# Kernel optimization log

Measured on AMD Instinct MI355X. Metric: run time of the kernel, lower is better.

Reference implementation:

```python
import jax, jax.numpy as jnp
import numpy as np

DIRECTIONS = [(0, 0), (1, 0), (-1, 0), (0, 1), (0, -1)]  # (dx, dy)
BN_EPS = 1e-5


def shift2d(x, directions=DIRECTIONS):
    # x: (B, C, H, W). Split channels into G groups, roll each spatially,
    # zero out the wrapped-around border (zero_pad mode), then concat.
    C = x.shape[1]
    G = len(directions)
    base = C // G
    sizes = [base] * (G - 1) + [C - base * (G - 1)]
    starts = np.concatenate([[0], np.cumsum(sizes)])
    out = []
    for i, (dx, dy) in enumerate(directions):
        chunk = x[:, starts[i]:starts[i + 1]]
        if dx == 0 and dy == 0:
            out.append(chunk)
            continue
        y = jnp.roll(chunk, shift=(dy, dx), axis=(-2, -1))
        if dy > 0:
            y = y.at[..., :dy, :].set(0.0)
        elif dy < 0:
            y = y.at[..., dy:, :].set(0.0)
        if dx > 0:
            y = y.at[..., :, :dx].set(0.0)
        elif dx < 0:
            y = y.at[..., :, dx:].set(0.0)
        out.append(y)
    return jnp.concatenate(out, axis=1)


def setup_inputs() -> dict:
    key = jax.random.key(0)
    k1, k2, k3, k4 = jax.random.split(key, 4)
    B, Cin, Cout, H, W = 32, 256, 256, 56, 56
    x = jax.random.normal(k1, (B, Cin, H, W), dtype=jnp.float32)
    pw_w = jax.random.normal(k2, (Cout, Cin), dtype=jnp.float32) * (1.0 / np.sqrt(Cin))
    gamma = jnp.ones((Cout,), dtype=jnp.float32)
    beta = jnp.zeros((Cout,), dtype=jnp.float32)
    running_mean = jax.random.normal(k3, (Cout,), dtype=jnp.float32) * 0.1
    running_var = jax.random.uniform(k4, (Cout,), dtype=jnp.float32, minval=0.5, maxval=1.5)
    return {"x": x, "pw_w": pw_w, "gamma": gamma, "beta": beta,
            "running_mean": running_mean, "running_var": running_var}


def reference(x, pw_w, gamma, beta, running_mean, running_var):
    # Shift (parameter-free spatial mixing)
    y = shift2d(x)
    # stride=1 -> down is Identity
    # 1x1 conv (no bias): pointwise channel mixing
    y = jnp.einsum('bchw,oc->bohw', y, pw_w)
    # BatchNorm2d (inference form with running stats) + ReLU
    inv = gamma * jax.lax.rsqrt(running_var + BN_EPS)
    y = y * inv[None, :, None, None] + (beta - running_mean * inv)[None, :, None, None]
    return jax.nn.relu(y)
```

## Files before the change

kernel.cpp:

```cpp
#include <hip/hip_runtime.h>

#define H_ 56
#define W_ 56
#define HW_ 3136
#define CIN_ 256
#define COUT_ 256

typedef __attribute__((ext_vector_type(8))) short short8;
typedef __attribute__((ext_vector_type(4))) float f32x4;

__device__ unsigned short g_wbf[COUT_ * CIN_];

__device__ __forceinline__ int swz32(int n) { return ((n ^ (n >> 3)) & 3) << 3; }

__device__ __forceinline__ unsigned short f2bf(float f) {
  union { float f; unsigned int i; } v; v.f = f;
  unsigned int b = v.i + (0x7fffu + ((v.i >> 16) & 1u));
  return (unsigned short)(b >> 16);
}

__device__ __forceinline__ void gload_lds16(const unsigned short* g, unsigned short* l) {
  __builtin_amdgcn_global_load_lds(
      (const __attribute__((address_space(1))) unsigned int*)g,
      (__attribute__((address_space(3))) unsigned int*)l, 16, 0, 0);
}

__device__ __forceinline__ void shift_decode(int c, int& dx, int& dy) {
  if (c < 102)      { dy = 0; dx = (c < 51) ? 0 : 1; }
  else if (c < 153) { dx = -1; dy = 0; }
  else if (c < 204) { dx = 0;  dy = 1; }
  else              { dx = 0;  dy = -1; }
}

__global__ __launch_bounds__(256)
void prep_weights(const float* __restrict__ wgt) {
  int idx  = blockIdx.x * 256 + threadIdx.x;
  int tile = idx >> 12;
  int bm = tile >> 3, kt = tile & 7;
  int e   = idx & 4095;
  int m   = e >> 5, col = e & 31;
  int o   = bm * 128 + m;
  int k   = kt * 32 + (col ^ swz32(m));
  g_wbf[idx] = f2bf(wgt[o * CIN_ + k]);
}

__global__ __launch_bounds__(256, 4)
void shiftconv_gemm(const float* __restrict__ x,
                    const float* __restrict__ gamma,
                    const float* __restrict__ beta,
                    const float* __restrict__ rmean,
                    const float* __restrict__ rvar,
                    float* __restrict__ out)
{
  __shared__ unsigned short Alds[2][128 * 32];
  __shared__ unsigned short Blds[2][64 * 32];
  __shared__ float bnp[256];

  const int t = threadIdx.x;
  const int orig = blockIdx.x;
  const int wgid = (orig & 7) * 392 + (orig >> 3);
  const int bm   = wgid & 1;
  const int bn   = wgid >> 1;

  const int lane = t & 63;
  const int wv   = t >> 6;
  const int wm   = wv >> 1;
  const int wn   = wv & 1;
  const int quad = lane >> 4;
  const int l15  = lane & 15;

  if (t < 128) {
    int o = bm * 128 + t;
    float inv = gamma[o] * rsqrtf(rvar[o] + 1e-5f);
    bnp[2 * t]     = inv;
    bnp[2 * t + 1] = beta[o] - rmean[o] * inv;
  }

  const int nl    = t & 63;
  const int kk    = (t >> 6) * 8;
  const int nglob = bn * 64 + nl;
  const int bidx  = nglob / HW_;
  const int rem   = nglob - bidx * HW_;
  const int hh    = rem / W_;
  const int ww    = rem - hh * W_;
  const size_t xb = (size_t)bidx * CIN_ * HW_;
  unsigned short* bdst0 = &Blds[0][nl * 32 + (kk ^ swz32(nl))];
  unsigned short* bdst1 = &Blds[1][nl * 32 + (kk ^ swz32(nl))];

  const unsigned short* wsrc = g_wbf + bm * (8 * 4096) + t * 8;

  f32x4 acc[4][2];
  #pragma unroll
  for (int i = 0; i < 4; ++i)
    #pragma unroll
    for (int j = 0; j < 2; ++j)
      acc[i][j] = (f32x4){0.f, 0.f, 0.f, 0.f};

  float fv[8];

  auto loadB = [&](int ktile) {
    #pragma unroll
    for (int j = 0; j < 8; ++j) {
      int c = ktile * 32 + kk + j;
      int dx, dy; shift_decode(c, dx, dy);
      int h2 = hh - dy, w2 = ww - dx;
      float v = 0.f;
      if ((unsigned)h2 < (unsigned)H_ && (unsigned)w2 < (unsigned)W_)
        v = x[xb + (size_t)c * HW_ + h2 * W_ + w2];
      fv[j] = v;
    }
  };
  auto writeB = [&](unsigned short* dst) {
    union { short8 v; unsigned short s[8]; } pk;
    #pragma unroll
    for (int j = 0; j < 8; ++j) pk.s[j] = f2bf(fv[j]);
    *(short8*)dst = pk.v;
  };

  {
    const unsigned short* g = wsrc;
    gload_lds16(g,        &Alds[0][wv * 512]);
    gload_lds16(g + 2048, &Alds[0][wv * 512 + 2048]);
  }
  loadB(0);
  writeB(bdst0);
  __syncthreads();

  const int kb = quad * 8;
  int buf = 0;

  for (int kt = 0; kt < 8; ++kt) {
    if (kt < 7) {
      const unsigned short* g = wsrc + (kt + 1) * 4096;
      gload_lds16(g,        &Alds[buf ^ 1][wv * 512]);
      gload_lds16(g + 2048, &Alds[buf ^ 1][wv * 512 + 2048]);
      loadB(kt + 1);
    }

    short8 af[4], bfr[2];
    #pragma unroll
    for (int f = 0; f < 4; ++f) {
      int ml = wm * 64 + f * 16 + l15;
      af[f] = *(const short8*)(&Alds[buf][ml * 32 + (kb ^ swz32(ml))]);
    }
    #pragma unroll
    for (int g2 = 0; g2 < 2; ++g2) {
      int nl2 = wn * 32 + g2 * 16 + l15;
      bfr[g2] = *(const short8*)(&Blds[buf][nl2 * 32 + (kb ^ swz32(nl2))]);
    }
    #pragma unroll
    for (int mf = 0; mf < 4; ++mf)
      #pragma unroll
      for (int nf = 0; nf < 2; ++nf)
        acc[mf][nf] = __builtin_amdgcn_mfma_f32_16x16x32_bf16(
            af[mf], bfr[nf], acc[mf][nf], 0, 0, 0);

    if (kt < 7)
      writeB((buf ^ 1) ? bdst1 : bdst0);

    __syncthreads();
    buf ^= 1;
  }

  size_t nbase[2];
  #pragma unroll
  for (int nf = 0; nf < 2; ++nf) {
    int ng  = bn * 64 + wn * 32 + nf * 16 + l15;
    int b2  = ng / HW_;
    int hw2 = ng - b2 * HW_;
    nbase[nf] = (size_t)b2 * COUT_ * HW_ + hw2;
  }
  #pragma unroll
  for (int mf = 0; mf < 4; ++mf) {
    int mloc = wm * 64 + mf * 16 + quad * 4;
    float inv[4], add[4];
    #pragma unroll
    for (int r = 0; r < 4; ++r) {
      inv[r] = bnp[2 * (mloc + r)];
      add[r] = bnp[2 * (mloc + r) + 1];
    }
    size_t obase = (size_t)(bm * 128 + mloc) * HW_;
    #pragma unroll
    for (int nf = 0; nf < 2; ++nf) {
      #pragma unroll
      for (int r = 0; r < 4; ++r) {
        float v = fmaf(acc[mf][nf][r], inv[r], add[r]);
        out[nbase[nf] + obase + (size_t)r * HW_] = fmaxf(v, 0.0f);
      }
    }
  }
}

extern "C" void kernel_launch(void* const* d_in, const int* in_sizes, int n_in,
                              void* d_out, int out_size, void* d_ws, size_t ws_size,
                              hipStream_t stream) {
  const float* x     = (const float*)d_in[0];
  const float* wgt   = (const float*)d_in[1];
  const float* gamma = (const float*)d_in[2];
  const float* beta  = (const float*)d_in[3];
  const float* rmean = (const float*)d_in[4];
  const float* rvar  = (const float*)d_in[5];
  float* out = (float*)d_out;

  prep_weights<<<dim3(256), dim3(256), 0, stream>>>(wgt);
  shiftconv_gemm<<<dim3(3136), dim3(256), 0, stream>>>(x, gamma, beta, rmean, rvar, out);
}
```

Measured before the change: 210.7 us.

## Double K tile to 64, restructure shifted B loads with precomputed masks

```diff
diff --git a/kernel.cpp b/kernel.cpp
--- a/kernel.cpp
+++ b/kernel.cpp
@@ -11,8 +11,6 @@
 
 __device__ unsigned short g_wbf[COUT_ * CIN_];
 
-__device__ __forceinline__ int swz32(int n) { return ((n ^ (n >> 3)) & 3) << 3; }
-
 __device__ __forceinline__ unsigned short f2bf(float f) {
   union { float f; unsigned int i; } v; v.f = f;
   unsigned int b = v.i + (0x7fffu + ((v.i >> 16) & 1u));
@@ -25,26 +23,26 @@
       (__attribute__((address_space(3))) unsigned int*)l, 16, 0, 0);
 }
 
-__device__ __forceinline__ void shift_decode(int c, int& dx, int& dy) {
-  if (c < 102)      { dy = 0; dx = (c < 51) ? 0 : 1; }
-  else if (c < 153) { dx = -1; dy = 0; }
-  else if (c < 204) { dx = 0;  dy = 1; }
-  else              { dx = 0;  dy = -1; }
-}
-
 __global__ __launch_bounds__(256)
 void prep_weights(const float* __restrict__ wgt) {
-  int idx  = blockIdx.x * 256 + threadIdx.x;
-  int tile = idx >> 12;
-  int bm = tile >> 3, kt = tile & 7;
-  int e   = idx & 4095;
-  int m   = e >> 5, col = e & 31;
+  int idx = blockIdx.x * 256 + threadIdx.x;
+  int bm  = idx >> 15;
+  int kt  = (idx >> 13) & 3;
+  int e   = idx & 8191;
+  int m   = e >> 6;
+  int u   = (e >> 3) & 7;
+  int j   = e & 7;
   int o   = bm * 128 + m;
-  int k   = kt * 32 + (col ^ swz32(m));
+  int k   = kt * 64 + (((u ^ (m & 7)) << 3) | j);
   g_wbf[idx] = f2bf(wgt[o * CIN_ + k]);
 }
 
-__global__ __launch_bounds__(256, 4)
+__device__ __forceinline__ float shload(const float* __restrict__ p, bool m, int off) {
+  float v = p[m ? off : 0];
+  return m ? v : 0.f;
+}
+
+__global__ __launch_bounds__(256, 3)
 void shiftconv_gemm(const float* __restrict__ x,
                     const float* __restrict__ gamma,
                     const float* __restrict__ beta,
@@ -52,8 +50,8 @@
                     const float* __restrict__ rvar,
                     float* __restrict__ out)
 {
-  __shared__ unsigned short Alds[2][128 * 32];
-  __shared__ unsigned short Blds[2][64 * 32];
+  __shared__ unsigned short Alds[2][128 * 64];
+  __shared__ unsigned short Blds[2][64 * 64];
   __shared__ float bnp[256];
 
   const int t = threadIdx.x;
@@ -77,17 +75,23 @@
   }
 
   const int nl    = t & 63;
-  const int kk    = (t >> 6) * 8;
+  const int kg    = __builtin_amdgcn_readfirstlane(t >> 6);
+  const int kg16  = kg << 4;
   const int nglob = bn * 64 + nl;
   const int bidx  = nglob / HW_;
   const int rem   = nglob - bidx * HW_;
   const int hh    = rem / W_;
   const int ww    = rem - hh * W_;
-  const size_t xb = (size_t)bidx * CIN_ * HW_;
-  unsigned short* bdst0 = &Blds[0][nl * 32 + (kk ^ swz32(nl))];
-  unsigned short* bdst1 = &Blds[1][nl * 32 + (kk ^ swz32(nl))];
-
-  const unsigned short* wsrc = g_wbf + bm * (8 * 4096) + t * 8;
+  const float* __restrict__ px = x + (size_t)bidx * CIN_ * HW_ + hh * W_ + ww;
+  const bool mL = (ww >= 1);
+  const bool mR = (ww <= W_ - 2);
+  const bool mU = (hh >= 1);
+  const bool mD = (hh <= H_ - 2);
+  const int  h7 = nl & 7;
+  unsigned short* const bpA = &Blds[0][nl * 64];
+  unsigned short* const bpB = &Blds[1][nl * 64];
+
+  const unsigned short* wsrc = g_wbf + bm * 32768 + t * 8;
 
   f32x4 acc[4][2];
   #pragma unroll
@@ -96,67 +100,76 @@
     for (int j = 0; j < 2; ++j)
       acc[i][j] = (f32x4){0.f, 0.f, 0.f, 0.f};
 
-  float fv[8];
-
-  auto loadB = [&](int ktile) {
-    #pragma unroll
-    for (int j = 0; j < 8; ++j) {
-      int c = ktile * 32 + kk + j;
-      int dx, dy; shift_decode(c, dx, dy);
-      int h2 = hh - dy, w2 = ww - dx;
-      float v = 0.f;
-      if ((unsigned)h2 < (unsigned)H_ && (unsigned)w2 < (unsigned)W_)
-        v = x[xb + (size_t)c * HW_ + h2 * W_ + w2];
+  float fv[16];
+
+  auto loadB = [&](int kt4) {
+    #pragma unroll
+    for (int j = 0; j < 16; ++j) {
+      int c = kt4 * 64 + kg16 + j;
+      const float* p = px + (size_t)c * HW_;
+      float v;
+      if (c < 51)       v = p[0];
+      else if (c < 102) v = shload(p, mL, -1);
+      else if (c < 153) v = shload(p, mR, +1);
+      else if (c < 204) v = shload(p, mU, -W_);
+      else              v = shload(p, mD, +W_);
       fv[j] = v;
     }
   };
-  auto writeB = [&](unsigned short* dst) {
-    union { short8 v; unsigned short s[8]; } pk;
-    #pragma unroll
-    for (int j = 0; j < 8; ++j) pk.s[j] = f2bf(fv[j]);
-    *(short8*)dst = pk.v;
+  auto writeB = [&](unsigned short* bp) {
+    union { short8 v; unsigned short s[8]; } pa, pb;
+    #pragma unroll
+    for (int j = 0; j < 8; ++j) { pa.s[j] = f2bf(fv[j]); pb.s[j] = f2bf(fv[8 + j]); }
+    int s0 = kg * 2;
+    *(short8*)(bp + (((s0    ) ^ h7) << 3)) = pa.v;
+    *(short8*)(bp + (((s0 | 1) ^ h7) << 3)) = pb.v;
   };
-
-  {
-    const unsigned short* g = wsrc;
-    gload_lds16(g,        &Alds[0][wv * 512]);
-    gload_lds16(g + 2048, &Alds[0][wv * 512 + 2048]);
-  }
+  auto stageA = [&](int bsel, int kt4) {
+    const unsigned short* g = wsrc + kt4 * 8192;
+    unsigned short* l = &Alds[bsel][t * 8];
+    gload_lds16(g,        l);
+    gload_lds16(g + 2048, l + 2048);
+    gload_lds16(g + 4096, l + 4096);
+    gload_lds16(g + 6144, l + 6144);
+  };
+
+  stageA(0, 0);
   loadB(0);
-  writeB(bdst0);
+  writeB(bpA);
   __syncthreads();
 
-  const int kb = quad * 8;
   int buf = 0;
 
-  for (int kt = 0; kt < 8; ++kt) {
-    if (kt < 7) {
-      const unsigned short* g = wsrc + (kt + 1) * 4096;
-      gload_lds16(g,        &Alds[buf ^ 1][wv * 512]);
-      gload_lds16(g + 2048, &Alds[buf ^ 1][wv * 512 + 2048]);
+  for (int kt = 0; kt < 4; ++kt) {
+    if (kt < 3) {
+      stageA(buf ^ 1, kt + 1);
       loadB(kt + 1);
     }
 
-    short8 af[4], bfr[2];
-    #pragma unroll
-    for (int f = 0; f < 4; ++f) {
-      int ml = wm * 64 + f * 16 + l15;
-      af[f] = *(const short8*)(&Alds[buf][ml * 32 + (kb ^ swz32(ml))]);
-    }
-    #pragma unroll
-    for (int g2 = 0; g2 < 2; ++g2) {
-      int nl2 = wn * 32 + g2 * 16 + l15;
-      bfr[g2] = *(const short8*)(&Blds[buf][nl2 * 32 + (kb ^ swz32(nl2))]);
-    }
-    #pragma unroll
-    for (int mf = 0; mf < 4; ++mf)
-      #pragma unroll
-      for (int nf = 0; nf < 2; ++nf)
-        acc[mf][nf] = __builtin_amdgcn_mfma_f32_16x16x32_bf16(
-            af[mf], bfr[nf], acc[mf][nf], 0, 0, 0);
-
-    if (kt < 7)
-      writeB((buf ^ 1) ? bdst1 : bdst0);
+    #pragma unroll
+    for (int ks = 0; ks < 2; ++ks) {
+      const int sA = ks * 4 + quad;
+      short8 af[4], bfr[2];
+      #pragma unroll
+      for (int f = 0; f < 4; ++f) {
+        int ml = wm * 64 + f * 16 + l15;
+        af[f] = *(const short8*)(&Alds[buf][ml * 64 + ((sA ^ (ml & 7)) << 3)]);
+      }
+      #pragma unroll
+      for (int g2 = 0; g2 < 2; ++g2) {
+        int nl2 = wn * 32 + g2 * 16 + l15;
+        bfr[g2] = *(const short8*)(&Blds[buf][nl2 * 64 + ((sA ^ (nl2 & 7)) << 3)]);
+      }
+      #pragma unroll
+      for (int mf = 0; mf < 4; ++mf)
+        #pragma unroll
+        for (int nf = 0; nf < 2; ++nf)
+          acc[mf][nf] = __builtin_amdgcn_mfma_f32_16x16x32_bf16(
+              af[mf], bfr[nf], acc[mf][nf], 0, 0, 0);
+    }
+
+    if (kt < 3)
+      writeB((buf ^ 1) ? bpB : bpA);
 
     __syncthreads();
     buf ^= 1;
```

Result: slower. 330.0 us (+56.6%).
